# Optimization experiments

Measured on AMD Instinct MI355X. Metric: run time of the kernel, lower is better.

Reference implementation:

```python
import jax, jax.numpy as jnp
import numpy as np

N_BALL = 256
N_EDGES = N_BALL * (N_BALL - 1)  # fully connected, no self loops
BATCH = 4
F_IN = 64
H = 64  # out_channels
EDGE_TYPES = 2


def _edge_structure():
    # receiver repeated pattern / sender covering all other nodes, as in NRI
    recv, send = [], []
    for r in range(N_BALL):
        for s in range(N_BALL):
            if s != r:
                recv.append(r)
                send.append(s)
    eye = np.eye(N_BALL, dtype=np.float32)
    rel_rec = eye[np.array(recv)]   # [E, N]
    rel_send = eye[np.array(send)]  # [E, N]
    return jnp.asarray(rel_rec), jnp.asarray(rel_send)


def setup_inputs() -> dict:
    key = jax.random.key(0)
    ks = jax.random.split(key, 12)
    rel_rec, rel_send = _edge_structure()
    s1 = 1.0 / np.sqrt(2 * F_IN)
    s2 = 1.0 / np.sqrt(H)
    s3 = 1.0 / np.sqrt(F_IN + H)
    return {
        "inputs": jax.random.normal(ks[0], (BATCH, N_BALL, F_IN), jnp.float32),
        "rel_type": jax.random.uniform(ks[1], (BATCH, N_EDGES, EDGE_TYPES), jnp.float32),
        "rel_rec": rel_rec,
        "rel_send": rel_send,
        # per-edge-type message MLPs (stacked over edge types)
        "W1": jax.random.uniform(ks[2], (EDGE_TYPES, 2 * F_IN, H), jnp.float32, -s1, s1),
        "b1": jax.random.uniform(ks[3], (EDGE_TYPES, H), jnp.float32, -s1, s1),
        "W2": jax.random.uniform(ks[4], (EDGE_TYPES, H, H), jnp.float32, -s2, s2),
        "b2": jax.random.uniform(ks[5], (EDGE_TYPES, H), jnp.float32, -s2, s2),
        # output MLP
        "Wo1": jax.random.uniform(ks[6], (F_IN + H, H), jnp.float32, -s3, s3),
        "bo1": jax.random.uniform(ks[7], (H,), jnp.float32, -s3, s3),
        "Wo2": jax.random.uniform(ks[8], (H, H), jnp.float32, -s2, s2),
        "bo2": jax.random.uniform(ks[9], (H,), jnp.float32, -s2, s2),
    }


def reference(inputs, rel_type, rel_rec, rel_send, W1, b1, W2, b2, Wo1, bo1, Wo2, bo2):
    # gather node features onto edges via one-hot matmuls
    receivers = jnp.einsum('en,bnf->bef', rel_rec, inputs)   # [B,E,F]
    senders = jnp.einsum('en,bnf->bef', rel_send, inputs)    # [B,E,F]
    pre_msg = jnp.concatenate([senders, receivers], axis=-1)  # [B,E,2F]

    all_msgs = jnp.zeros(pre_msg.shape[:2] + (H,), dtype=pre_msg.dtype)
    for i in range(EDGE_TYPES):  # skip_first=False -> start at 0
        msg = jax.nn.relu(pre_msg @ W1[i] + b1[i])
        msg = jax.nn.relu(msg @ W2[i] + b2[i])
        all_msgs = all_msgs + msg * rel_type[:, :, i:i + 1]

    # scatter-aggregate edge messages back to receiver nodes
    agg_msgs = jnp.einsum('beh,en->bnh', all_msgs, rel_rec)   # [B,N,H]
    aug_inputs = jnp.concatenate([inputs, agg_msgs], axis=-1)  # [B,N,F+H]

    pred = jax.nn.relu(aug_inputs @ Wo1 + bo1)
    pred = jax.nn.relu(pred @ Wo2 + bo2)
    return inputs + pred
```

## Files before the change

### kernel.cpp

```cpp
#include <hip/hip_runtime.h>
#include <hip/hip_bf16.h>

#define BATCH 4
#define NB    256
#define NE    (NB*(NB-1))

typedef short  short8  __attribute__((ext_vector_type(8)));
typedef float  f32x16  __attribute__((ext_vector_type(16)));

__device__ __forceinline__ short f2bf(float x) {
    __hip_bfloat16 h = __float2bfloat16(x);
    return __builtin_bit_cast(short, h);
}
__device__ __forceinline__ float bf2f(short s) {
    unsigned u = ((unsigned)(unsigned short)s) << 16;
    return __builtin_bit_cast(float, u);
}

__global__ __launch_bounds__(256) void prep_kernel(
    const float* __restrict__ x,
    const float* __restrict__ W1,
    const float* __restrict__ b1,
    const float* __restrict__ W2,
    const float* __restrict__ Wo1,
    const float* __restrict__ Wo2,
    short* __restrict__ Pbf,
    float* __restrict__ Q,
    short* __restrict__ W2f,
    float* __restrict__ Wo1T,
    float* __restrict__ Wo2T)
{
    __shared__ float xl[4][64];
    const int blk = blockIdx.x;
    const int t   = threadIdx.x;

    if (blk < 512) {
        const int i   = blk >> 8;
        const int rem = blk & 255;
        const int b   = rem >> 6;
        const int g   = t >> 6;
        const int n   = (rem & 63) * 4 + g;
        const int h   = t & 63;
        xl[g][h] = x[(b * NB + n) * 64 + h];
        __syncthreads();
        const float* w1s = W1 + i * 8192;
        const float* w1r = w1s + 4096;
        float accP = 0.f;
        float accQ = b1[i * 64 + h];
        #pragma unroll 16
        for (int f = 0; f < 64; ++f) {
            const float xv = xl[g][f];
            accP = fmaf(xv, w1s[f * 64 + h], accP);
            accQ = fmaf(xv, w1r[f * 64 + h], accQ);
        }
        Pbf[(((i * BATCH + b) * 8 + (h >> 3)) * NB + n) * 8 + (h & 7)] = f2bf(accP);
        Q[((i * BATCH + b) * NB + n) * 64 + h] = accQ;
    } else if (blk == 512) {
        #pragma unroll
        for (int q = 0; q < 32; ++q) {
            const int e  = q * 256 + t;
            const int j  = e & 7, ln = (e >> 3) & 63, k0 = (e >> 9) & 3,
                      nt = (e >> 11) & 1, i = e >> 12;
            const int k  = k0 * 16 + 8 * (ln >> 5) + j;
            const int n  = (ln & 31) + 32 * nt;
            W2f[e] = f2bf(W2[(i * 64 + k) * 64 + n]);
        }
    } else if (blk == 513) {
        #pragma unroll
        for (int q = 0; q < 32; ++q) {
            const int e = q * 256 + t;
            Wo1T[e] = Wo1[(e & 127) * 64 + (e >> 7)];
        }
    } else {
        #pragma unroll
        for (int q = 0; q < 16; ++q) {
            const int e = q * 256 + t;
            Wo2T[e] = Wo2[(e & 63) * 64 + (e >> 6)];
        }
    }
}

__global__ __launch_bounds__(256) void main_kernel(
    const float* __restrict__ x,
    const float* __restrict__ rel_type,
    const float* __restrict__ b2,
    const float* __restrict__ bo1,
    const float* __restrict__ bo2,
    const short* __restrict__ Pbf,
    const float* __restrict__ Q,
    const short* __restrict__ W2f,
    const float* __restrict__ Wo1T,
    const float* __restrict__ Wo2T,
    float* __restrict__ out)
{
    const int b = blockIdx.x >> 8;
    const int r = blockIdx.x & 255;
    const int t = threadIdx.x;
    const int lane = t & 63;
    const int w    = t >> 6;
    const int l31  = lane & 31;
    const int lh   = lane >> 5;

    __shared__ __align__(16) float rt[256][2];
    __shared__ __align__(16) float qrow[2][64];
    __shared__ __align__(16) float b2l[2][64];
    __shared__ __align__(16) short W2l[8192];
    __shared__ __align__(16) float red[4][64];
    __shared__ __align__(16) float xl[64];
    __shared__ __align__(16) float aggl[64];
    __shared__ __align__(16) float predl[64];

    if (t < 255) {
        const float* p = rel_type + ((size_t)b * NE + (size_t)r * 255 + t) * 2;
        rt[t][0] = p[0];
        rt[t][1] = p[1];
    } else {
        rt[255][0] = 0.f; rt[255][1] = 0.f;
    }
    #pragma unroll
    for (int q = 0; q < 4; ++q) {
        const int e = (q * 256 + t) * 8;
        *(short8*)(W2l + e) = *(const short8*)(W2f + e);
    }
    if (t < 128) {
        const int i = t >> 6, h = t & 63;
        qrow[i][h] = Q[((i * BATCH + b) * NB + r) * 64 + h];
        b2l[i][h]  = b2[i * 64 + h];
    }
    if (t >= 128 && t < 192) xl[t - 128] = x[(b * NB + r) * 64 + (t - 128)];
    __syncthreads();

    const int k0m = 64 * w + l31;
    const int k1m = k0m + 32;
    int s0 = (k0m < r) ? k0m : k0m + 1; if (s0 > 255) s0 = 255;
    int s1 = (k1m < r) ? k1m : k1m + 1; if (s1 > 255) s1 = 255;

    float psum0 = 0.f, psum1 = 0.f;

    #pragma unroll
    for (int i = 0; i < 2; ++i) {
        const short* Pb = Pbf + (size_t)(i * BATCH + b) * (8 * NB * 8);

        short8 L0[4], L1[4];
        #pragma unroll
        for (int k0 = 0; k0 < 4; ++k0) {
            const int hb = 2 * k0 + lh;
            L0[k0] = *(const short8*)(Pb + (hb * NB + s0) * 8);
            L1[k0] = *(const short8*)(Pb + (hb * NB + s1) * 8);
        }

        f32x16 acc00 = {}, acc01 = {}, acc10 = {}, acc11 = {};
        #pragma unroll
        for (int k0 = 0; k0 < 4; ++k0) {
            const int h0 = (2 * k0 + lh) * 8;
            short8 a0, a1;
            #pragma unroll
            for (int e = 0; e < 8; ++e) {
                const float qv = qrow[i][h0 + e];
                a0[e] = f2bf(fmaxf(bf2f(L0[k0][e]) + qv, 0.f));
                a1[e] = f2bf(fmaxf(bf2f(L1[k0][e]) + qv, 0.f));
            }
            const short8 B0 = *(const short8*)(W2l + ((i * 8 + k0) * 64 + lane) * 8);
            const short8 B1 = *(const short8*)(W2l + ((i * 8 + 4 + k0) * 64 + lane) * 8);
            acc00 = __builtin_amdgcn_mfma_f32_32x32x16_bf16(a0, B0, acc00, 0, 0, 0);
            acc01 = __builtin_amdgcn_mfma_f32_32x32x16_bf16(a0, B1, acc01, 0, 0, 0);
            acc10 = __builtin_amdgcn_mfma_f32_32x32x16_bf16(a1, B0, acc10, 0, 0, 0);
            acc11 = __builtin_amdgcn_mfma_f32_32x32x16_bf16(a1, B1, acc11, 0, 0, 0);
        }

        const float b2v0 = b2l[i][l31];
        const float b2v1 = b2l[i][l31 + 32];
        #pragma unroll
        for (int reg = 0; reg < 16; ++reg) {
            const int rowoff = (reg & 3) + 8 * (reg >> 2) + 4 * lh;
            const float rt0 = rt[64 * w + rowoff][i];
            const float rt1 = rt[64 * w + 32 + rowoff][i];
            psum0 += fmaxf(acc00[reg] + b2v0, 0.f) * rt0;
            psum1 += fmaxf(acc01[reg] + b2v1, 0.f) * rt0;
            psum0 += fmaxf(acc10[reg] + b2v0, 0.f) * rt1;
            psum1 += fmaxf(acc11[reg] + b2v1, 0.f) * rt1;
        }
    }

    float4 wv1[8];
    #pragma unroll
    for (int q = 0; q < 8; ++q)
        wv1[q] = *(const float4*)(Wo1T + lane * 128 + w * 32 + q * 4);
    float4 wv2[4];
    #pragma unroll
    for (int q = 0; q < 4; ++q)
        wv2[q] = *(const float4*)(Wo2T + lane * 64 + w * 16 + q * 4);

    psum0 += __shfl_xor(psum0, 32, 64);
    psum1 += __shfl_xor(psum1, 32, 64);
    if (lh == 0) {
        red[w][l31]      = psum0;
        red[w][l31 + 32] = psum1;
    }
    __syncthreads();
    if (t < 64) aggl[t] = red[0][t] + red[1][t] + red[2][t] + red[3][t];
    __syncthreads();

    {
        const float* src = (w < 2) ? (xl + w * 32) : (aggl + (w - 2) * 32);
        float s = 0.f;
        #pragma unroll
        for (int q = 0; q < 8; ++q)
            #pragma unroll
            for (int e = 0; e < 4; ++e)
                s = fmaf(src[q * 4 + e], wv1[q][e], s);
        red[w][lane] = s;
    }
    __syncthreads();
    if (t < 64)
        predl[t] = fmaxf(red[0][t] + red[1][t] + red[2][t] + red[3][t] + bo1[t], 0.f);
    __syncthreads();

    {
        float s = 0.f;
        #pragma unroll
        for (int q = 0; q < 4; ++q)
            #pragma unroll
            for (int e = 0; e < 4; ++e)
                s = fmaf(predl[w * 16 + q * 4 + e], wv2[q][e], s);
        red[w][lane] = s;
    }
    __syncthreads();
    if (t < 64)
        out[((size_t)b * NB + r) * 64 + t] =
            xl[t] + fmaxf(red[0][t] + red[1][t] + red[2][t] + red[3][t] + bo2[t], 0.f);
}

extern "C" void kernel_launch(void* const* d_in, const int* in_sizes, int n_in,
                              void* d_out, int out_size, void* d_ws, size_t ws_size,
                              hipStream_t stream) {
    (void)in_sizes; (void)n_in; (void)out_size; (void)ws_size;

    const float* x    = (const float*)d_in[0];
    const float* rt   = (const float*)d_in[1];
    const float* W1   = (const float*)d_in[4];
    const float* b1   = (const float*)d_in[5];
    const float* W2   = (const float*)d_in[6];
    const float* b2   = (const float*)d_in[7];
    const float* Wo1  = (const float*)d_in[8];
    const float* bo1  = (const float*)d_in[9];
    const float* Wo2  = (const float*)d_in[10];
    const float* bo2  = (const float*)d_in[11];
    float* out = (float*)d_out;

    char* ws = (char*)d_ws;
    short* Pbf  = (short*)ws;
    float* Q    = (float*)(ws + 262144);
    short* W2f  = (short*)(ws + 786432);
    float* Wo1T = (float*)(ws + 802816);
    float* Wo2T = (float*)(ws + 835584);

    prep_kernel<<<515, 256, 0, stream>>>(x, W1, b1, W2, Wo1, Wo2,
                                         Pbf, Q, W2f, Wo1T, Wo2T);
    main_kernel<<<BATCH * NB, 256, 0, stream>>>(x, rt, b2, bo1, bo2,
                                                Pbf, Q, W2f, Wo1T, Wo2T, out);
}
```

Measured before the change: 26.98 us.

## Fuse prep into main kernel and compute sender projection per block with MFMA

Drops the separate prep kernel. Each block now converts the whole batch's node features to bf16 in swizzled LDS, then computes the sender half of the first MLP layer with MFMA, seeding the accumulator with the receiver projection. Layer-1 outputs are repacked into layer-2 A fragments in registers with permlane32 swaps. W2 conversion and the Wo1/Wo2 reads move inline, which removes a launch and the workspace round-trip. The cost is that every block redoes the W1 sender projection and the W2 conversion, and uses more LDS and registers.

```diff
diff --git a/kernel.cpp b/kernel.cpp
--- a/kernel.cpp
+++ b/kernel.cpp
@@ -5,191 +5,205 @@
 #define NB    256
 #define NE    (NB*(NB-1))
 
-typedef short  short8  __attribute__((ext_vector_type(8)));
-typedef float  f32x16  __attribute__((ext_vector_type(16)));
+typedef short    short8 __attribute__((ext_vector_type(8)));
+typedef float    f32x16 __attribute__((ext_vector_type(16)));
+typedef unsigned u32x4  __attribute__((ext_vector_type(4)));
 
 __device__ __forceinline__ short f2bf(float x) {
-    __hip_bfloat16 h = __float2bfloat16(x);
-    return __builtin_bit_cast(short, h);
-}
-__device__ __forceinline__ float bf2f(short s) {
-    unsigned u = ((unsigned)(unsigned short)s) << 16;
-    return __builtin_bit_cast(float, u);
-}
-
-__global__ __launch_bounds__(256) void prep_kernel(
+    return __builtin_bit_cast(short, __float2bfloat16(x));
+}
+__device__ __forceinline__ unsigned pk2(float lo, float hi) {
+    return (unsigned)(unsigned short)f2bf(lo) |
+           ((unsigned)(unsigned short)f2bf(hi) << 16);
+}
+__device__ __forceinline__ void pl32swap(unsigned& a, unsigned& b) {
+    asm volatile("v_permlane32_swap_b32 %0, %1" : "+v"(a), "+v"(b));
+}
+
+__device__ __forceinline__ void loadA1(const float* __restrict__ W1i,
+                                       int l31, int lh, short8 a1f[2][4]) {
+    #pragma unroll
+    for (int ht = 0; ht < 2; ++ht)
+        #pragma unroll
+        for (int k0 = 0; k0 < 4; ++k0) {
+            const int h  = l31 + 32 * ht;
+            const int fb = 16 * k0 + 8 * lh;
+            short8 v;
+            #pragma unroll
+            for (int j = 0; j < 8; ++j) v[j] = f2bf(W1i[(fb + j) * 64 + h]);
+            a1f[ht][k0] = v;
+        }
+}
+
+__global__ __launch_bounds__(256, 3) void fused_kernel(
     const float* __restrict__ x,
+    const float* __restrict__ rel_type,
     const float* __restrict__ W1,
     const float* __restrict__ b1,
     const float* __restrict__ W2,
+    const float* __restrict__ b2,
     const float* __restrict__ Wo1,
+    const float* __restrict__ bo1,
     const float* __restrict__ Wo2,
-    short* __restrict__ Pbf,
-    float* __restrict__ Q,
-    short* __restrict__ W2f,
-    float* __restrict__ Wo1T,
-    float* __restrict__ Wo2T)
-{
-    __shared__ float xl[4][64];
-    const int blk = blockIdx.x;
-    const int t   = threadIdx.x;
-
-    if (blk < 512) {
-        const int i   = blk >> 8;
-        const int rem = blk & 255;
-        const int b   = rem >> 6;
-        const int g   = t >> 6;
-        const int n   = (rem & 63) * 4 + g;
-        const int h   = t & 63;
-        xl[g][h] = x[(b * NB + n) * 64 + h];
-        __syncthreads();
-        const float* w1s = W1 + i * 8192;
-        const float* w1r = w1s + 4096;
-        float accP = 0.f;
-        float accQ = b1[i * 64 + h];
-        #pragma unroll 16
-        for (int f = 0; f < 64; ++f) {
-            const float xv = xl[g][f];
-            accP = fmaf(xv, w1s[f * 64 + h], accP);
-            accQ = fmaf(xv, w1r[f * 64 + h], accQ);
-        }
-        Pbf[(((i * BATCH + b) * 8 + (h >> 3)) * NB + n) * 8 + (h & 7)] = f2bf(accP);
-        Q[((i * BATCH + b) * NB + n) * 64 + h] = accQ;
-    } else if (blk == 512) {
-        #pragma unroll
-        for (int q = 0; q < 32; ++q) {
-            const int e  = q * 256 + t;
-            const int j  = e & 7, ln = (e >> 3) & 63, k0 = (e >> 9) & 3,
-                      nt = (e >> 11) & 1, i = e >> 12;
-            const int k  = k0 * 16 + 8 * (ln >> 5) + j;
-            const int n  = (ln & 31) + 32 * nt;
-            W2f[e] = f2bf(W2[(i * 64 + k) * 64 + n]);
-        }
-    } else if (blk == 513) {
-        #pragma unroll
-        for (int q = 0; q < 32; ++q) {
-            const int e = q * 256 + t;
-            Wo1T[e] = Wo1[(e & 127) * 64 + (e >> 7)];
-        }
-    } else {
-        #pragma unroll
-        for (int q = 0; q < 16; ++q) {
-            const int e = q * 256 + t;
-            Wo2T[e] = Wo2[(e & 63) * 64 + (e >> 6)];
-        }
-    }
-}
-
-__global__ __launch_bounds__(256) void main_kernel(
-    const float* __restrict__ x,
-    const float* __restrict__ rel_type,
-    const float* __restrict__ b2,
-    const float* __restrict__ bo1,
     const float* __restrict__ bo2,
-    const short* __restrict__ Pbf,
-    const float* __restrict__ Q,
-    const short* __restrict__ W2f,
-    const float* __restrict__ Wo1T,
-    const float* __restrict__ Wo2T,
     float* __restrict__ out)
 {
-    const int b = blockIdx.x >> 8;
-    const int r = blockIdx.x & 255;
-    const int t = threadIdx.x;
+    const int b    = blockIdx.x >> 8;
+    const int r    = blockIdx.x & 255;
+    const int t    = threadIdx.x;
     const int lane = t & 63;
     const int w    = t >> 6;
     const int l31  = lane & 31;
     const int lh   = lane >> 5;
 
-    __shared__ __align__(16) float rt[256][2];
+    __shared__ __align__(16) short xbf[NB * 64];
+    __shared__ __align__(16) short W2l[8192];
+    __shared__ __align__(16) float rt2[2][256];
     __shared__ __align__(16) float qrow[2][64];
-    __shared__ __align__(16) float b2l[2][64];
-    __shared__ __align__(16) short W2l[8192];
     __shared__ __align__(16) float red[4][64];
     __shared__ __align__(16) float xl[64];
     __shared__ __align__(16) float aggl[64];
     __shared__ __align__(16) float predl[64];
 
+    short8 a1f[2][4];
+    loadA1(W1, l31, lh, a1f);
+
+    const float* xb = x + (size_t)b * NB * 64;
+    #pragma unroll
+    for (int rep = 0; rep < 4; ++rep) {
+        const int n  = (t >> 2) + 64 * rep;
+        const int f0 = (t & 3) * 16;
+        float4 v0 = *(const float4*)(xb + n * 64 + f0);
+        float4 v1 = *(const float4*)(xb + n * 64 + f0 + 4);
+        float4 v2 = *(const float4*)(xb + n * 64 + f0 + 8);
+        float4 v3 = *(const float4*)(xb + n * 64 + f0 + 12);
+        short8 s0 = { f2bf(v0.x), f2bf(v0.y), f2bf(v0.z), f2bf(v0.w),
+                      f2bf(v1.x), f2bf(v1.y), f2bf(v1.z), f2bf(v1.w) };
+        short8 s1 = { f2bf(v2.x), f2bf(v2.y), f2bf(v2.z), f2bf(v2.w),
+                      f2bf(v3.x), f2bf(v3.y), f2bf(v3.z), f2bf(v3.w) };
+        const int base = n * 128;
+        const int sw   = (n & 7) << 4;
+        *(short8*)((char*)xbf + (base + ((f0 * 2)      ^ sw))) = s0;
+        *(short8*)((char*)xbf + (base + ((f0 * 2 + 16) ^ sw))) = s1;
+    }
     if (t < 255) {
         const float* p = rel_type + ((size_t)b * NE + (size_t)r * 255 + t) * 2;
-        rt[t][0] = p[0];
-        rt[t][1] = p[1];
+        rt2[0][t] = p[0];
+        rt2[1][t] = p[1];
     } else {
-        rt[255][0] = 0.f; rt[255][1] = 0.f;
-    }
-    #pragma unroll
-    for (int q = 0; q < 4; ++q) {
-        const int e = (q * 256 + t) * 8;
-        *(short8*)(W2l + e) = *(const short8*)(W2f + e);
-    }
+        rt2[0][255] = 0.f; rt2[1][255] = 0.f;
+    }
+    if (t >= 192) xl[t - 192] = xb[r * 64 + (t - 192)];
+    __syncthreads();
+
     if (t < 128) {
         const int i = t >> 6, h = t & 63;
-        qrow[i][h] = Q[((i * BATCH + b) * NB + r) * 64 + h];
-        b2l[i][h]  = b2[i * 64 + h];
-    }
-    if (t >= 128 && t < 192) xl[t - 128] = x[(b * NB + r) * 64 + (t - 128)];
-    __syncthreads();
-
-    const int k0m = 64 * w + l31;
-    const int k1m = k0m + 32;
-    int s0 = (k0m < r) ? k0m : k0m + 1; if (s0 > 255) s0 = 255;
-    int s1 = (k1m < r) ? k1m : k1m + 1; if (s1 > 255) s1 = 255;
+        float acc = b1[i * 64 + h];
+        const float* w1r = W1 + i * 8192 + 4096;
+        #pragma unroll 16
+        for (int f = 0; f < 64; ++f) acc = fmaf(xl[f], w1r[f * 64 + h], acc);
+        qrow[i][h] = acc;
+    } else {
+        const int i  = (t >> 6) - 2;
+        const int ln = t & 63;
+        #pragma unroll
+        for (int c = 0; c < 8; ++c) {
+            const int nt = c >> 2, k0 = c & 3;
+            short8 v;
+            #pragma unroll
+            for (int j = 0; j < 8; ++j) {
+                const int k = 16 * k0 + 8 * (ln >> 5) + j;
+                const int n = (ln & 31) + 32 * nt;
+                v[j] = f2bf(W2[(i * 64 + k) * 64 + n]);
+            }
+            *(short8*)(W2l + ((i * 8 + c) * 64 + ln) * 8) = v;
+        }
+    }
+    __syncthreads();
+
+    short8 b1f[2][4];
+    #pragma unroll
+    for (int et = 0; et < 2; ++et) {
+        const int kap = 64 * w + 32 * et + l31;
+        int s = (kap < r) ? kap : kap + 1;
+        if (s > 255) s = 255;
+        const int base = s * 128, sw = (s & 7) << 4;
+        #pragma unroll
+        for (int k0 = 0; k0 < 4; ++k0)
+            b1f[et][k0] = *(const short8*)((const char*)xbf +
+                              (base + (((32 * k0 + 16 * lh)) ^ sw)));
+    }
+
+    const float bv[2][2] = { { b2[l31], b2[32 + l31] },
+                             { b2[64 + l31], b2[96 + l31] } };
 
     float psum0 = 0.f, psum1 = 0.f;
 
     #pragma unroll
     for (int i = 0; i < 2; ++i) {
-        const short* Pb = Pbf + (size_t)(i * BATCH + b) * (8 * NB * 8);
-
-        short8 L0[4], L1[4];
-        #pragma unroll
-        for (int k0 = 0; k0 < 4; ++k0) {
-            const int hb = 2 * k0 + lh;
-            L0[k0] = *(const short8*)(Pb + (hb * NB + s0) * 8);
-            L1[k0] = *(const short8*)(Pb + (hb * NB + s1) * 8);
-        }
-
-        f32x16 acc00 = {}, acc01 = {}, acc10 = {}, acc11 = {};
-        #pragma unroll
-        for (int k0 = 0; k0 < 4; ++k0) {
-            const int h0 = (2 * k0 + lh) * 8;
-            short8 a0, a1;
-            #pragma unroll
-            for (int e = 0; e < 8; ++e) {
-                const float qv = qrow[i][h0 + e];
-                a0[e] = f2bf(fmaxf(bf2f(L0[k0][e]) + qv, 0.f));
-                a1[e] = f2bf(fmaxf(bf2f(L1[k0][e]) + qv, 0.f));
-            }
-            const short8 B0 = *(const short8*)(W2l + ((i * 8 + k0) * 64 + lane) * 8);
-            const short8 B1 = *(const short8*)(W2l + ((i * 8 + 4 + k0) * 64 + lane) * 8);
-            acc00 = __builtin_amdgcn_mfma_f32_32x32x16_bf16(a0, B0, acc00, 0, 0, 0);
-            acc01 = __builtin_amdgcn_mfma_f32_32x32x16_bf16(a0, B1, acc01, 0, 0, 0);
-            acc10 = __builtin_amdgcn_mfma_f32_32x32x16_bf16(a1, B0, acc10, 0, 0, 0);
-            acc11 = __builtin_amdgcn_mfma_f32_32x32x16_bf16(a1, B1, acc11, 0, 0, 0);
-        }
-
-        const float b2v0 = b2l[i][l31];
-        const float b2v1 = b2l[i][l31 + 32];
-        #pragma unroll
-        for (int reg = 0; reg < 16; ++reg) {
-            const int rowoff = (reg & 3) + 8 * (reg >> 2) + 4 * lh;
-            const float rt0 = rt[64 * w + rowoff][i];
-            const float rt1 = rt[64 * w + 32 + rowoff][i];
-            psum0 += fmaxf(acc00[reg] + b2v0, 0.f) * rt0;
-            psum1 += fmaxf(acc01[reg] + b2v1, 0.f) * rt0;
-            psum0 += fmaxf(acc10[reg] + b2v0, 0.f) * rt1;
-            psum1 += fmaxf(acc11[reg] + b2v1, 0.f) * rt1;
-        }
-    }
-
-    float4 wv1[8];
-    #pragma unroll
-    for (int q = 0; q < 8; ++q)
-        wv1[q] = *(const float4*)(Wo1T + lane * 128 + w * 32 + q * 4);
-    float4 wv2[4];
-    #pragma unroll
-    for (int q = 0; q < 4; ++q)
-        wv2[q] = *(const float4*)(Wo2T + lane * 64 + w * 16 + q * 4);
+        short8 a2f[2][4];
+        #pragma unroll
+        for (int et = 0; et < 2; ++et) {
+            f32x16 acc1[2];
+            #pragma unroll
+            for (int ht = 0; ht < 2; ++ht) {
+                f32x16 a;
+                #pragma unroll
+                for (int qd = 0; qd < 4; ++qd) {
+                    float4 qq = *(const float4*)(&qrow[i][32 * ht + 8 * qd + 4 * lh]);
+                    a[4 * qd] = qq.x; a[4 * qd + 1] = qq.y;
+                    a[4 * qd + 2] = qq.z; a[4 * qd + 3] = qq.w;
+                }
+                #pragma unroll
+                for (int k0 = 0; k0 < 4; ++k0)
+                    a = __builtin_amdgcn_mfma_f32_32x32x16_bf16(a1f[ht][k0],
+                                                                b1f[et][k0], a, 0, 0, 0);
+                acc1[ht] = a;
+            }
+            #pragma unroll
+            for (int k0 = 0; k0 < 4; ++k0) {
+                const int ht = k0 >> 1;
+                const int qa = 2 * (k0 & 1), qb = qa + 1;
+                unsigned a0 = pk2(fmaxf(acc1[ht][4 * qa], 0.f),
+                                  fmaxf(acc1[ht][4 * qa + 1], 0.f));
+                unsigned a1 = pk2(fmaxf(acc1[ht][4 * qa + 2], 0.f),
+                                  fmaxf(acc1[ht][4 * qa + 3], 0.f));
+                unsigned b0 = pk2(fmaxf(acc1[ht][4 * qb], 0.f),
+                                  fmaxf(acc1[ht][4 * qb + 1], 0.f));
+                unsigned b1w = pk2(fmaxf(acc1[ht][4 * qb + 2], 0.f),
+                                   fmaxf(acc1[ht][4 * qb + 3], 0.f));
+                pl32swap(a0, b0);
+                pl32swap(a1, b1w);
+                u32x4 fw = { a0, a1, b0, b1w };
+                a2f[et][k0] = __builtin_bit_cast(short8, fw);
+            }
+        }
+
+        if (i == 0) loadA1(W1 + 8192, l31, lh, a1f);
+
+        #pragma unroll
+        for (int et = 0; et < 2; ++et) {
+            f32x16 acc20, acc21;
+            #pragma unroll
+            for (int e = 0; e < 16; ++e) { acc20[e] = bv[i][0]; acc21[e] = bv[i][1]; }
+            #pragma unroll
+            for (int k0 = 0; k0 < 4; ++k0) {
+                const short8 B0 = *(const short8*)(W2l + ((i * 8 + k0) * 64 + lane) * 8);
+                const short8 B1 = *(const short8*)(W2l + ((i * 8 + 4 + k0) * 64 + lane) * 8);
+                acc20 = __builtin_amdgcn_mfma_f32_32x32x16_bf16(a2f[et][k0], B0, acc20, 0, 0, 0);
+                acc21 = __builtin_amdgcn_mfma_f32_32x32x16_bf16(a2f[et][k0], B1, acc21, 0, 0, 0);
+            }
+            #pragma unroll
+            for (int qd = 0; qd < 4; ++qd) {
+                float4 rq = *(const float4*)(&rt2[i][64 * w + 32 * et + 8 * qd + 4 * lh]);
+                #pragma unroll
+                for (int m = 0; m < 4; ++m) {
+                    psum0 += fmaxf(acc20[4 * qd + m], 0.f) * rq[m];
+                    psum1 += fmaxf(acc21[4 * qd + m], 0.f) * rq[m];
+                }
+            }
+        }
+    }
 
     psum0 += __shfl_xor(psum0, 32, 64);
     psum1 += __shfl_xor(psum1, 32, 64);
@@ -203,12 +217,10 @@
 
     {
         const float* src = (w < 2) ? (xl + w * 32) : (aggl + (w - 2) * 32);
+        const float* Wp  = Wo1 + (w * 32) * 64 + lane;
         float s = 0.f;
-        #pragma unroll
-        for (int q = 0; q < 8; ++q)
-            #pragma unroll
-            for (int e = 0; e < 4; ++e)
-                s = fmaf(src[q * 4 + e], wv1[q][e], s);
+        #pragma unroll 8
+        for (int jj = 0; jj < 32; ++jj) s = fmaf(src[jj], Wp[jj * 64], s);
         red[w][lane] = s;
     }
     __syncthreads();
@@ -217,12 +229,10 @@
     __syncthreads();
 
     {
+        const float* Wp = Wo2 + (w * 16) * 64 + lane;
         float s = 0.f;
         #pragma unroll
-        for (int q = 0; q < 4; ++q)
-            #pragma unroll
-            for (int e = 0; e < 4; ++e)
-                s = fmaf(predl[w * 16 + q * 4 + e], wv2[q][e], s);
+        for (int jj = 0; jj < 16; ++jj) s = fmaf(predl[w * 16 + jj], Wp[jj * 64], s);
         red[w][lane] = s;
     }
     __syncthreads();
@@ -234,7 +244,7 @@
 extern "C" void kernel_launch(void* const* d_in, const int* in_sizes, int n_in,
                               void* d_out, int out_size, void* d_ws, size_t ws_size,
                               hipStream_t stream) {
-    (void)in_sizes; (void)n_in; (void)out_size; (void)ws_size;
+    (void)in_sizes; (void)n_in; (void)out_size; (void)d_ws; (void)ws_size;
 
     const float* x    = (const float*)d_in[0];
     const float* rt   = (const float*)d_in[1];
@@ -248,15 +258,6 @@
     const float* bo2  = (const float*)d_in[11];
     float* out = (float*)d_out;
 
-    char* ws = (char*)d_ws;
-    short* Pbf  = (short*)ws;
-    float* Q    = (float*)(ws + 262144);
-    short* W2f  = (short*)(ws + 786432);
-    float* Wo1T = (float*)(ws + 802816);
-    float* Wo2T = (float*)(ws + 835584);
-
-    prep_kernel<<<515, 256, 0, stream>>>(x, W1, b1, W2, Wo1, Wo2,
-                                         Pbf, Q, W2f, Wo1T, Wo2T);
-    main_kernel<<<BATCH * NB, 256, 0, stream>>>(x, rt, b2, bo1, bo2,
-                                                Pbf, Q, W2f, Wo1T, Wo2T, out);
-}
+    fused_kernel<<<BATCH * NB, 256, 0, stream>>>(x, rt, W1, b1, W2, b2,
+                                                 Wo1, bo1, Wo2, bo2, out);
+}
```

Result: slower. 40.77 us (+51.1%).
